# Performance work log

Measured on AMD Instinct MI355X. Metric: run time of the kernel, lower is better.

Reference implementation:

```python
import jax, jax.numpy as jnp
import numpy as np

N_NODES = 50000
N_EDGES = 800000
D = 64
L = 3


def setup_inputs() -> dict:
    key = jax.random.key(0)
    ks = jax.random.split(key, 6)
    glorot = (6.0 / (D + D)) ** 0.5  # xavier_uniform bound for [D,D]
    return {
        "x": jax.random.normal(ks[0], (N_NODES, D), dtype=jnp.float32),
        "edge_index": jax.random.randint(ks[1], (2, N_EDGES), 0, N_NODES, dtype=jnp.int32),
        "edge_weight": jax.random.uniform(ks[2], (N_EDGES,), dtype=jnp.float32),
        "W_rel": jax.random.uniform(ks[3], (L, D, D), jnp.float32, -glorot, glorot),
        "b_rel": jnp.zeros((L, D), dtype=jnp.float32),
        "W_root": jax.random.uniform(ks[4], (L, D, D), jnp.float32, -glorot, glorot),
    }


def reference(x, edge_index, edge_weight, W_rel, b_rel, W_root):
    """myGNN_hidden.full_forward final embedding: L GraphConv(add) layers, tanh on last.
    GraphConv: h_i' = h_i @ W_root + (sum_{j->i} e_ji * h_j) @ W_rel + b_rel.
    """
    src, dst = edge_index[0], edge_index[1]
    n = x.shape[0]
    h = x
    num_layers = W_rel.shape[0]
    for i in range(num_layers):
        msg = edge_weight[:, None] * h[src]                      # [E, D] gather + scale
        agg = jax.ops.segment_sum(msg, dst, num_segments=n)      # [N, D] scatter-add
        h = agg @ W_rel[i] + b_rel[i] + h @ W_root[i]
        if i == num_layers - 1:
            h = jnp.tanh(h)
    return h
```

## Files before the change

### kernel.cpp

```cpp
#include <hip/hip_runtime.h>
#include <hip/hip_bf16.h>

#define NN 50000
#define NE 800000
#define DD 64
#define NL 3

__device__ __forceinline__ int rlanei(int v, int l) {
    return __builtin_amdgcn_readlane(v, l);
}
__device__ __forceinline__ float rlane(float v, int l) {
    return __int_as_float(__builtin_amdgcn_readlane(__float_as_int(v), l));
}

__global__ void hist_kernel(const int* __restrict__ dst, int* __restrict__ deg) {
    int t = blockIdx.x * blockDim.x + threadIdx.x;
    int e = t * 4;
    if (e + 4 <= NE) {
        int4 d4 = *reinterpret_cast<const int4*>(dst + e);
        atomicAdd(&deg[d4.x], 1);
        atomicAdd(&deg[d4.y], 1);
        atomicAdd(&deg[d4.z], 1);
        atomicAdd(&deg[d4.w], 1);
    } else {
        for (int i = e; i < NE; ++i) atomicAdd(&deg[dst[i]], 1);
    }
}

__global__ void alloc_kernel(const int* __restrict__ deg,
                             int* __restrict__ row_start,
                             int* __restrict__ cursor,
                             int* __restrict__ counter) {
    int n = blockIdx.x * blockDim.x + threadIdx.x;
    int lane = threadIdx.x & 63;
    int d = (n < NN) ? deg[n] : 0;
    int s = d;
    #pragma unroll
    for (int off = 1; off < 64; off <<= 1) {
        int t = __shfl_up(s, off);
        if (lane >= off) s += t;
    }
    int total = __shfl(s, 63);
    int base = 0;
    if (lane == 63) base = atomicAdd(counter, total);
    base = __shfl(base, 63);
    int my = base + s - d;
    if (n < NN) { row_start[n] = my; cursor[n] = my; }
}

__global__ void reorder_kernel(const int* __restrict__ src,
                               const int* __restrict__ dst,
                               const float* __restrict__ w,
                               int* __restrict__ cursor,
                               int2* __restrict__ e_sw) {
    int t = blockIdx.x * blockDim.x + threadIdx.x;
    int e = t * 2;
    if (e + 2 <= NE) {
        int2   s2 = *reinterpret_cast<const int2*>(src + e);
        int2   d2 = *reinterpret_cast<const int2*>(dst + e);
        float2 w2 = *reinterpret_cast<const float2*>(w + e);
        int p0 = atomicAdd(&cursor[d2.x], 1);
        e_sw[p0] = make_int2(s2.x, __float_as_int(w2.x));
        int p1 = atomicAdd(&cursor[d2.y], 1);
        e_sw[p1] = make_int2(s2.y, __float_as_int(w2.y));
    } else {
        for (int i = e; i < NE; ++i) {
            int p = atomicAdd(&cursor[dst[i]], 1);
            e_sw[p] = make_int2(src[i], __float_as_int(w[i]));
        }
    }
}

template<bool LAST>
__global__ void __launch_bounds__(256, 3)
fused_kernel(const float* __restrict__ h,
             const int* __restrict__ row_start,
             const int* __restrict__ deg,
             const int2* __restrict__ e_sw,
             const float* __restrict__ Wrel,
             const float* __restrict__ Wroot,
             const float* __restrict__ b,
             float* __restrict__ hout) {
    const int lane   = threadIdx.x & 63;
    const int wgid   = __builtin_amdgcn_readfirstlane((int)((blockIdx.x * blockDim.x + threadIdx.x) >> 6));
    const int nwaves = (gridDim.x * blockDim.x) >> 6;

    float w1[DD], w2[DD];
    #pragma unroll
    for (int k = 0; k < DD; ++k) {
        w1[k] = Wrel[k * DD + lane];
        w2[k] = Wroot[k * DD + lane];
    }
    const float bias = b[lane];

    for (int n = wgid; n < NN; n += nwaves) {
        const int beg = row_start[n];
        const int dg  = deg[n];
        const int end = beg + dg;

        float g0 = 0.f, g1 = 0.f, g2 = 0.f, g3 = 0.f;
        for (int i = beg; i < end; i += 64) {
            int cnt = min(64, end - i);
            int2 e = make_int2(0, 0);
            if (i + lane < end) e = e_sw[i + lane];
            int vs = e.x, vw = e.y;
            int j = 0;
            for (; j + 4 <= cnt; j += 4) {
                int   s0 = rlanei(vs, j+0); float f0 = __int_as_float(rlanei(vw, j+0));
                int   s1 = rlanei(vs, j+1); float f1 = __int_as_float(rlanei(vw, j+1));
                int   s2 = rlanei(vs, j+2); float f2 = __int_as_float(rlanei(vw, j+2));
                int   s3 = rlanei(vs, j+3); float f3 = __int_as_float(rlanei(vw, j+3));
                g0 += f0 * h[(size_t)s0 * DD + lane];
                g1 += f1 * h[(size_t)s1 * DD + lane];
                g2 += f2 * h[(size_t)s2 * DD + lane];
                g3 += f3 * h[(size_t)s3 * DD + lane];
            }
            for (; j < cnt; ++j) {
                int s0 = rlanei(vs, j); float f0 = __int_as_float(rlanei(vw, j));
                g0 += f0 * h[(size_t)s0 * DD + lane];
            }
        }
        const float vagg = (g0 + g1) + (g2 + g3);
        const float vh   = h[(size_t)n * DD + lane];

        float a0 = bias, a1 = 0.f, a2 = 0.f, a3 = 0.f;
        #pragma unroll
        for (int k = 0; k < DD; k += 2) {
            float sa0 = rlane(vagg, k),     sh0 = rlane(vh, k);
            float sa1 = rlane(vagg, k + 1), sh1 = rlane(vh, k + 1);
            a0 += sa0 * w1[k];
            a1 += sh0 * w2[k];
            a2 += sa1 * w1[k + 1];
            a3 += sh1 * w2[k + 1];
        }
        float r = (a0 + a1) + (a2 + a3);
        if (LAST) r = tanhf(r);
        hout[(size_t)n * DD + lane] = r;
    }
}

extern "C" void kernel_launch(void* const* d_in, const int* in_sizes, int n_in,
                              void* d_out, int out_size, void* d_ws, size_t ws_size,
                              hipStream_t stream) {
    const float* x     = (const float*)d_in[0];
    const int*   ei    = (const int*)d_in[1];
    const float* ew    = (const float*)d_in[2];
    const float* Wrel  = (const float*)d_in[3];
    const float* brel  = (const float*)d_in[4];
    const float* Wroot = (const float*)d_in[5];
    float* out = (float*)d_out;

    float* hA        = (float*)d_ws;
    float* hB        = hA + (size_t)NN * DD;
    int2*  e_sw      = (int2*)(hB + (size_t)NN * DD);
    int*   row_start = (int*)(e_sw + NE);
    int*   cursor    = row_start + NN;
    int*   deg       = cursor + NN;
    int*   counter   = deg + NN;

    const int* src = ei;
    const int* dst = ei + NE;

    const int hblocks = (NE / 4 + 255) / 256;
    const int rblocks = (NE / 2 + 255) / 256;
    const int ablocks = (NN + 255) / 256;
    const int fblocks = 1536;

    hipMemsetAsync(deg, 0, (size_t)(NN + 1) * sizeof(int), stream);
    hist_kernel<<<hblocks, 256, 0, stream>>>(dst, deg);
    alloc_kernel<<<ablocks, 256, 0, stream>>>(deg, row_start, cursor, counter);
    reorder_kernel<<<rblocks, 256, 0, stream>>>(src, dst, ew, cursor, e_sw);

    fused_kernel<false><<<fblocks, 256, 0, stream>>>(x,  row_start, deg, e_sw, Wrel,           Wroot,           brel,        hA);
    fused_kernel<false><<<fblocks, 256, 0, stream>>>(hA, row_start, deg, e_sw, Wrel + DD*DD,   Wroot + DD*DD,   brel + DD,   hB);
    fused_kernel<true ><<<fblocks, 256, 0, stream>>>(hB, row_start, deg, e_sw, Wrel + 2*DD*DD, Wroot + 2*DD*DD, brel + 2*DD, out);
}
```

Baseline: 365.9 us.

## Split fused layer into separate gather and dense kernels

Each layer's fused gather+transform kernel is split in two. A high-occupancy gather kernel (one wave per node, 8 accumulators, scalar edge loads) writes the aggregate to a buffer, and a dense kernel holding the weight registers does the matmul. The aim is to free the latency-bound gather from the 128-register weight tiles that capped occupancy at 3 blocks per CU. The cost is an extra N×D write and read of the aggregate per layer, plus three more launches. The dense kernel writes hA in place, which is safe only because each wave reads its own row before writing it.

```diff
diff --git a/kernel.cpp b/kernel.cpp
--- a/kernel.cpp
+++ b/kernel.cpp
@@ -6,9 +6,6 @@
 #define DD 64
 #define NL 3
 
-__device__ __forceinline__ int rlanei(int v, int l) {
-    return __builtin_amdgcn_readlane(v, l);
-}
 __device__ __forceinline__ float rlane(float v, int l) {
     return __int_as_float(__builtin_amdgcn_readlane(__float_as_int(v), l));
 }
@@ -71,16 +68,48 @@
     }
 }
 
+__global__ void __launch_bounds__(256, 8)
+gather_kernel(const float* __restrict__ h,
+              const int* __restrict__ row_start,
+              const int* __restrict__ deg,
+              const int2* __restrict__ e_sw,
+              float* __restrict__ agg) {
+    int wid = (blockIdx.x * blockDim.x + threadIdx.x) >> 6;
+    if (wid >= NN) return;
+    int lane = threadIdx.x & 63;
+    int beg = row_start[wid];
+    int end = beg + deg[wid];
+    float a0=0.f,a1=0.f,a2=0.f,a3=0.f,a4=0.f,a5=0.f,a6=0.f,a7=0.f;
+    int i = beg;
+    for (; i + 8 <= end; i += 8) {
+        int2 e0 = e_sw[i+0]; int2 e1 = e_sw[i+1];
+        int2 e2 = e_sw[i+2]; int2 e3 = e_sw[i+3];
+        int2 e4 = e_sw[i+4]; int2 e5 = e_sw[i+5];
+        int2 e6 = e_sw[i+6]; int2 e7 = e_sw[i+7];
+        a0 += __int_as_float(e0.y) * h[(size_t)e0.x * DD + lane];
+        a1 += __int_as_float(e1.y) * h[(size_t)e1.x * DD + lane];
+        a2 += __int_as_float(e2.y) * h[(size_t)e2.x * DD + lane];
+        a3 += __int_as_float(e3.y) * h[(size_t)e3.x * DD + lane];
+        a4 += __int_as_float(e4.y) * h[(size_t)e4.x * DD + lane];
+        a5 += __int_as_float(e5.y) * h[(size_t)e5.x * DD + lane];
+        a6 += __int_as_float(e6.y) * h[(size_t)e6.x * DD + lane];
+        a7 += __int_as_float(e7.y) * h[(size_t)e7.x * DD + lane];
+    }
+    for (; i < end; ++i) {
+        int2 e = e_sw[i];
+        a0 += __int_as_float(e.y) * h[(size_t)e.x * DD + lane];
+    }
+    agg[(size_t)wid * DD + lane] = ((a0+a1)+(a2+a3)) + ((a4+a5)+(a6+a7));
+}
+
 template<bool LAST>
 __global__ void __launch_bounds__(256, 3)
-fused_kernel(const float* __restrict__ h,
-             const int* __restrict__ row_start,
-             const int* __restrict__ deg,
-             const int2* __restrict__ e_sw,
+dense_kernel(const float* __restrict__ agg,
+             const float* h,
              const float* __restrict__ Wrel,
              const float* __restrict__ Wroot,
              const float* __restrict__ b,
-             float* __restrict__ hout) {
+             float* hout) {
     const int lane   = threadIdx.x & 63;
     const int wgid   = __builtin_amdgcn_readfirstlane((int)((blockIdx.x * blockDim.x + threadIdx.x) >> 6));
     const int nwaves = (gridDim.x * blockDim.x) >> 6;
@@ -94,35 +123,8 @@
     const float bias = b[lane];
 
     for (int n = wgid; n < NN; n += nwaves) {
-        const int beg = row_start[n];
-        const int dg  = deg[n];
-        const int end = beg + dg;
-
-        float g0 = 0.f, g1 = 0.f, g2 = 0.f, g3 = 0.f;
-        for (int i = beg; i < end; i += 64) {
-            int cnt = min(64, end - i);
-            int2 e = make_int2(0, 0);
-            if (i + lane < end) e = e_sw[i + lane];
-            int vs = e.x, vw = e.y;
-            int j = 0;
-            for (; j + 4 <= cnt; j += 4) {
-                int   s0 = rlanei(vs, j+0); float f0 = __int_as_float(rlanei(vw, j+0));
-                int   s1 = rlanei(vs, j+1); float f1 = __int_as_float(rlanei(vw, j+1));
-                int   s2 = rlanei(vs, j+2); float f2 = __int_as_float(rlanei(vw, j+2));
-                int   s3 = rlanei(vs, j+3); float f3 = __int_as_float(rlanei(vw, j+3));
-                g0 += f0 * h[(size_t)s0 * DD + lane];
-                g1 += f1 * h[(size_t)s1 * DD + lane];
-                g2 += f2 * h[(size_t)s2 * DD + lane];
-                g3 += f3 * h[(size_t)s3 * DD + lane];
-            }
-            for (; j < cnt; ++j) {
-                int s0 = rlanei(vs, j); float f0 = __int_as_float(rlanei(vw, j));
-                g0 += f0 * h[(size_t)s0 * DD + lane];
-            }
-        }
-        const float vagg = (g0 + g1) + (g2 + g3);
+        const float vagg = agg[(size_t)n * DD + lane];
         const float vh   = h[(size_t)n * DD + lane];
-
         float a0 = bias, a1 = 0.f, a2 = 0.f, a3 = 0.f;
         #pragma unroll
         for (int k = 0; k < DD; k += 2) {
@@ -150,9 +152,9 @@
     const float* Wroot = (const float*)d_in[5];
     float* out = (float*)d_out;
 
-    float* hA        = (float*)d_ws;
-    float* hB        = hA + (size_t)NN * DD;
-    int2*  e_sw      = (int2*)(hB + (size_t)NN * DD);
+    float* agg       = (float*)d_ws;
+    float* hA        = agg + (size_t)NN * DD;
+    int2*  e_sw      = (int2*)(hA + (size_t)NN * DD);
     int*   row_start = (int*)(e_sw + NE);
     int*   cursor    = row_start + NN;
     int*   deg       = cursor + NN;
@@ -164,14 +166,18 @@
     const int hblocks = (NE / 4 + 255) / 256;
     const int rblocks = (NE / 2 + 255) / 256;
     const int ablocks = (NN + 255) / 256;
-    const int fblocks = 1536;
+    const int gblocks = (NN * 64 + 255) / 256;
+    const int dblocks = 1024;
 
     hipMemsetAsync(deg, 0, (size_t)(NN + 1) * sizeof(int), stream);
     hist_kernel<<<hblocks, 256, 0, stream>>>(dst, deg);
     alloc_kernel<<<ablocks, 256, 0, stream>>>(deg, row_start, cursor, counter);
     reorder_kernel<<<rblocks, 256, 0, stream>>>(src, dst, ew, cursor, e_sw);
 
-    fused_kernel<false><<<fblocks, 256, 0, stream>>>(x,  row_start, deg, e_sw, Wrel,           Wroot,           brel,        hA);
-    fused_kernel<false><<<fblocks, 256, 0, stream>>>(hA, row_start, deg, e_sw, Wrel + DD*DD,   Wroot + DD*DD,   brel + DD,   hB);
-    fused_kernel<true ><<<fblocks, 256, 0, stream>>>(hB, row_start, deg, e_sw, Wrel + 2*DD*DD, Wroot + 2*DD*DD, brel + 2*DD, out);
+    gather_kernel<<<gblocks, 256, 0, stream>>>(x, row_start, deg, e_sw, agg);
+    dense_kernel<false><<<dblocks, 256, 0, stream>>>(agg, x, Wrel, Wroot, brel, hA);
+    gather_kernel<<<gblocks, 256, 0, stream>>>(hA, row_start, deg, e_sw, agg);
+    dense_kernel<false><<<dblocks, 256, 0, stream>>>(agg, hA, Wrel + DD*DD, Wroot + DD*DD, brel + DD, hA);
+    gather_kernel<<<gblocks, 256, 0, stream>>>(hA, row_start, deg, e_sw, agg);
+    dense_kernel<true ><<<dblocks, 256, 0, stream>>>(agg, hA, Wrel + 2*DD*DD, Wroot + 2*DD*DD, brel + 2*DD, out);
 }
```

After: 362.1 us. No clear change (-1.0%).
